# Performance work log

Measured on AMD Instinct MI355X. Metric: run time of the kernel, lower is better.

The kernel has to match this reference:

```python
import jax, jax.numpy as jnp
import numpy as np

# dims: batch, seq, d_model, mlp_width, num_experts, lora_rank
B, S, D, M, E, R = 4, 1024, 2048, 5632, 8, 16
LORA_ALPHA = 32
SCALING = LORA_ALPHA / R  # = 2.0


def setup_inputs() -> dict:
    key = jax.random.key(0)
    ks = jax.random.split(key, 13)
    s = 0.02
    f32 = jnp.float32
    return {
        'x':  jax.random.normal(ks[0], (B, S, D), f32),
        # router: nn.Linear(d_model, num_experts)
        'Wr': jax.random.normal(ks[1], (E, D), f32) * s,
        'br': jax.random.normal(ks[2], (E,), f32) * s,
        # frozen original MLP weights (torch Linear layout [out, in])
        'Wg': jax.random.normal(ks[3], (M, D), f32) * s,
        'Wu': jax.random.normal(ks[4], (M, D), f32) * s,
        'Wd': jax.random.normal(ks[5], (D, M), f32) * s,
        # shared LoRA A matrices [rank, fan_in]
        'Ag': jax.random.normal(ks[6], (R, D), f32) * s,
        'Au': jax.random.normal(ks[7], (R, D), f32) * s,
        'Ad': jax.random.normal(ks[8], (R, M), f32) * s,
        # per-expert LoRA B matrices [E, fan_out, rank] (zero-init in the
        # original; randomized here so gradients/outputs are non-trivial)
        'Bg': jax.random.normal(ks[9], (E, M, R), f32) * s,
        'Bu': jax.random.normal(ks[10], (E, M, R), f32) * s,
        'Bd': jax.random.normal(ks[11], (E, D, R), f32) * s,
    }


def _lora_moe_dense(x, W, A, Bexp, routing):
    """Dense MoE LoRA: original_proj(x) + sum_e routing[...,e] * (x @ A^T @ B_e^T) * scaling.
    x: [b,s,in], W: [out,in], A: [r,in], Bexp: [E,out,r], routing: [b,s,E].
    Identical math to stacking all experts then weighted-summing, but the
    shared A lets us weight the tiny [b,s,E,r] hidden instead of [b,s,E,out].
    """
    orig = jnp.einsum('bsi,oi->bso', x, W)
    h = jnp.einsum('bsi,ri->bsr', x, A)            # shared low-rank hidden
    hw = jnp.einsum('bsr,bse->bser', h, routing)   # routing-weighted hidden
    lora = jnp.einsum('bser,eor->bso', hw, Bexp) * SCALING
    return orig + lora


def reference(x, Wr, br, Wg, Wu, Wd, Ag, Au, Ad, Bg, Bu, Bd):
    logits = jnp.einsum('bsd,ed->bse', x, Wr) + br
    routing = jax.nn.softmax(logits, axis=-1)
    idx = jnp.argmax(routing, axis=-1)
    y_hard = jax.nn.one_hot(idx, E, dtype=logits.dtype)
    # straight-through expert choice
    expert_choice = y_hard - jax.lax.stop_gradient(routing) + routing
    gate = _lora_moe_dense(x, Wg, Ag, Bg, routing)
    up = _lora_moe_dense(x, Wu, Au, Bu, routing)
    h = jax.nn.silu(gate) * up  # LLaMA-style SwiGLU act_fn
    out = _lora_moe_dense(h, Wd, Ad, Bd, routing)
    return out, routing, expert_choice
```

## Files before the change

### kernel.cpp

```cpp
#include <hip/hip_runtime.h>

#define DEV __device__ __forceinline__

typedef unsigned short u16;
typedef __bf16 bf16x8 __attribute__((ext_vector_type(8)));
typedef float f32x4 __attribute__((ext_vector_type(4)));

static DEV u16 f2bf(float f) {
    union { float f; unsigned u; } v; v.f = f;
    unsigned r = v.u + 0x7fffu + ((v.u >> 16) & 1u);
    return (u16)(r >> 16);
}
static DEV float bf2f(u16 u) {
    union { unsigned u; float f; } v; v.u = ((unsigned)u) << 16;
    return v.f;
}
static DEV void g2l16(const u16* g, u16* l) {
    __builtin_amdgcn_global_load_lds(
        (const __attribute__((address_space(1))) void*)g,
        (__attribute__((address_space(3))) void*)l, 16, 0, 0);
}


__global__ __launch_bounds__(256) void k_conv(
    const float* __restrict__ Wg, const float* __restrict__ Wu, const float* __restrict__ Wd,
    const float* __restrict__ Bg, const float* __restrict__ Bu, const float* __restrict__ Bd,
    u16* __restrict__ Wg16, u16* __restrict__ Wu16, u16* __restrict__ Wd16,
    u16* __restrict__ Bgx, u16* __restrict__ Bux, u16* __restrict__ Bdx)
{
    const long long NW = 2883584;
    const long long NB = 180224;
    const long long ND = 65536;
    long long gid = (long long)blockIdx.x * 256 + threadIdx.x;
    if (gid < 3 * NW) {
        const float* s; u16* d; long long g = gid;
        if (g < NW)           { s = Wg; d = Wg16; }
        else if (g < 2 * NW)  { s = Wu; d = Wu16; g -= NW; }
        else                  { s = Wd; d = Wd16; g -= 2 * NW; }
        float4 v = *(const float4*)(s + g * 4);
        ushort4 o; o.x = f2bf(v.x); o.y = f2bf(v.y); o.z = f2bf(v.z); o.w = f2bf(v.w);
        *(ushort4*)(d + g * 4) = o;
    } else {
        long long g = gid - 3 * NW;
        const float* s; u16* d; int nr;
        if (g < NB)               { s = Bg; d = Bgx; nr = 5632; }
        else if (g < 2 * NB)      { s = Bu; d = Bux; nr = 5632; g -= NB; }
        else if (g < 2 * NB + ND) { s = Bd; d = Bdx; nr = 2048; g -= 2 * NB; }
        else return;
        int n = (int)(g >> 5);
        int j0 = ((int)g & 31) * 4;
        int e = j0 >> 4, r0 = j0 & 15;
        float4 v = *(const float4*)&s[((size_t)e * nr + n) * 16 + r0];
        ushort4 o; o.x = f2bf(v.x); o.y = f2bf(v.y); o.z = f2bf(v.z); o.w = f2bf(v.w);
        *(ushort4*)&d[(size_t)n * 128 + j0] = o;
    }
}

__global__ __launch_bounds__(256) void k_router(
    const float* __restrict__ x, const float* __restrict__ Wr,
    const float* __restrict__ Ag, const float* __restrict__ Au,
    u16* __restrict__ x16, float* __restrict__ fin1)
{
    __shared__ float xs[64][65];
    __shared__ float wsm[40][64];
    const int rb = blockIdx.x, ksp = blockIdx.y;
    const int row0 = rb * 64;
    const int t = threadIdx.x;
    const int rloc = t & 63, og = t >> 6;
    float acc[10];
#pragma unroll
    for (int o = 0; o < 10; ++o) acc[o] = 0.f;

    for (int c4 = 0; c4 < 4; ++c4) {
        const int k0 = ksp * 256 + c4 * 64;
        __syncthreads();
#pragma unroll
        for (int i = 0; i < 4; ++i) {
            int idx = t + i * 256;
            int r = idx >> 4, c = (idx & 15) * 4;
            float4 v = *(const float4*)&x[(size_t)(row0 + r) * 2048 + k0 + c];
            xs[r][c + 0] = v.x; xs[r][c + 1] = v.y; xs[r][c + 2] = v.z; xs[r][c + 3] = v.w;
            ushort4 o; o.x = f2bf(v.x); o.y = f2bf(v.y); o.z = f2bf(v.z); o.w = f2bf(v.w);
            *(ushort4*)&x16[(size_t)(row0 + r) * 2048 + k0 + c] = o;
        }
#pragma unroll
        for (int i = 0; i < 3; ++i) {
            int idx = t + i * 256;
            if (idx < 640) {
                int r = idx >> 4, c = (idx & 15) * 4;
                const float* src = (r < 8) ? (Wr + (size_t)r * 2048)
                                : (r < 24) ? (Ag + (size_t)(r - 8) * 2048)
                                           : (Au + (size_t)(r - 24) * 2048);
                float4 v = *(const float4*)&src[k0 + c];
                wsm[r][c + 0] = v.x; wsm[r][c + 1] = v.y; wsm[r][c + 2] = v.z; wsm[r][c + 3] = v.w;
            }
        }
        __syncthreads();
#pragma unroll
        for (int k = 0; k < 64; ++k) {
            float xv = xs[rloc][k];
#pragma unroll
            for (int o = 0; o < 10; ++o) acc[o] += xv * wsm[og * 10 + o][k];
        }
    }
    float* dst = fin1 + ((size_t)ksp * 4096 + row0 + rloc) * 40 + og * 10;
#pragma unroll
    for (int o = 0; o < 10; ++o) dst[o] = acc[o];
}

__global__ __launch_bounds__(256) void k_fin1(
    const float* __restrict__ fin1, const float* __restrict__ br,
    float* __restrict__ routing_ws, float* __restrict__ out_rt, float* __restrict__ out_ec,
    u16* __restrict__ hwg, u16* __restrict__ hwu)
{
    const int row = blockIdx.x * 256 + threadIdx.x;
    float s[40];
#pragma unroll
    for (int j = 0; j < 40; ++j) s[j] = 0.f;
    for (int p = 0; p < 8; ++p) {
        const float* src = fin1 + ((size_t)p * 4096 + row) * 40;
#pragma unroll
        for (int j = 0; j < 40; ++j) s[j] += src[j];
    }
    float lg[8]; float m = -1e30f;
#pragma unroll
    for (int e = 0; e < 8; ++e) { lg[e] = s[e] + br[e]; m = fmaxf(m, lg[e]); }
    float ex[8]; float sum = 0.f;
#pragma unroll
    for (int e = 0; e < 8; ++e) { ex[e] = expf(lg[e] - m); sum += ex[e]; }
    float r8[8];
#pragma unroll
    for (int e = 0; e < 8; ++e) r8[e] = ex[e] / sum;
    int best = 0;
#pragma unroll
    for (int e = 1; e < 8; ++e) if (r8[e] > r8[best]) best = e;
#pragma unroll
    for (int e = 0; e < 8; ++e) {
        routing_ws[(size_t)row * 8 + e] = r8[e];
        out_rt[(size_t)row * 8 + e] = r8[e];
        float yh = (e == best) ? 1.f : 0.f;
        out_ec[(size_t)row * 8 + e] = (yh - r8[e]) + r8[e];
    }
#pragma unroll
    for (int e = 0; e < 8; ++e) {
        float re = r8[e];
#pragma unroll
        for (int rk = 0; rk < 16; ++rk) {
            hwg[(size_t)row * 128 + e * 16 + rk] = f2bf(2.f * s[8 + rk] * re);
            hwu[(size_t)row * 128 + e * 16 + rk] = f2bf(2.f * s[24 + rk] * re);
        }
    }
}

__global__ __launch_bounds__(256, 3) void k_gemm(
    const u16* __restrict__ A0, int lda0, const u16* __restrict__ A1,
    const u16* __restrict__ B0, int ldb0, const u16* __restrict__ B1,
    int Ksplit, int nkt, int MODE,
    float* __restrict__ outF, u16* __restrict__ outH, int ldc)
{
    __shared__ u16 As[128 * 64];
    __shared__ u16 Bs[128 * 64];
    const int t = threadIdx.x;
    const int lane = t & 63, wid = t >> 6;
    const int wr = wid >> 1, wc = wid & 1;
    const int row0 = blockIdx.x * 128, col0 = blockIdx.y * 128;

    f32x4 acc[4][4];
    const f32x4 zf = {0.f, 0.f, 0.f, 0.f};
#pragma unroll
    for (int i = 0; i < 4; ++i)
#pragma unroll
        for (int j = 0; j < 4; ++j) acc[i][j] = zf;

    for (int kt = 0; kt < nkt; ++kt) {
        const int k0 = kt * 64;
        const bool p2 = (k0 >= Ksplit);
        const u16* aS = p2 ? A1 : A0; const int aLd = p2 ? 128 : lda0; const int aC = p2 ? (k0 - Ksplit) : k0;
        const u16* bS = p2 ? B1 : B0; const int bLd = p2 ? 128 : ldb0; const int bC = p2 ? (k0 - Ksplit) : k0;
        __syncthreads();
#pragma unroll
        for (int i = 0; i < 4; ++i) {
            int idx = i * 256 + t;
            int r = idx >> 3, c = (idx & 7) * 8;
            g2l16(aS + (size_t)(row0 + r) * aLd + aC + c, &As[idx * 8]);
        }
#pragma unroll
        for (int i = 0; i < 4; ++i) {
            int idx = i * 256 + t;
            int r = idx >> 3, c = (idx & 7) * 8;
            g2l16(bS + (size_t)(col0 + r) * bLd + bC + c, &Bs[idx * 8]);
        }
        __syncthreads();
#pragma unroll
        for (int ks = 0; ks < 2; ++ks) {
            bf16x8 af[4], bfr[4];
#pragma unroll
            for (int fm = 0; fm < 4; ++fm)
                af[fm] = *(const bf16x8*)&As[(wr * 64 + fm * 16 + (lane & 15)) * 64 + ks * 32 + (lane >> 4) * 8];
#pragma unroll
            for (int fn = 0; fn < 4; ++fn)
                bfr[fn] = *(const bf16x8*)&Bs[(wc * 64 + fn * 16 + (lane & 15)) * 64 + ks * 32 + (lane >> 4) * 8];
#pragma unroll
            for (int fm = 0; fm < 4; ++fm)
#pragma unroll
                for (int fn = 0; fn < 4; ++fn)
                    acc[fm][fn] = __builtin_amdgcn_mfma_f32_16x16x32_bf16(af[fm], bfr[fn], acc[fm][fn], 0, 0, 0);
        }
    }

#pragma unroll
    for (int fm = 0; fm < 4; ++fm) {
#pragma unroll
        for (int fn = 0; fn < 4; ++fn) {
            const int col = col0 + wc * 64 + fn * 16 + (lane & 15);
            const int rowb = row0 + wr * 64 + fm * 16 + ((lane >> 4) << 2);
            f32x4 v = acc[fm][fn];
            if (MODE == 0) {
#pragma unroll
                for (int j = 0; j < 4; ++j) outF[(size_t)(rowb + j) * ldc + col] = v[j];
            } else if (MODE == 1) {
#pragma unroll
                for (int j = 0; j < 4; ++j) outH[(size_t)(rowb + j) * ldc + col] = f2bf(v[j]);
            } else {
#pragma unroll
                for (int j = 0; j < 4; ++j) {
                    size_t o = (size_t)(rowb + j) * ldc + col;
                    float g = bf2f(outH[o]);
                    float sg = g / (1.f + __expf(-g));
                    outH[o] = f2bf(sg * v[j]);
                }
            }
        }
    }
}

__global__ __launch_bounds__(256) void k_hd(
    const u16* __restrict__ h, const float* __restrict__ Ad, float* __restrict__ fin2)
{
    __shared__ float hs[64][65];
    __shared__ float as2[16][64];
    const int rb = blockIdx.x, ksp = blockIdx.y;
    const int row0 = rb * 64;
    const int t = threadIdx.x;
    const int rloc = t & 63, og = t >> 6;
    float acc[4] = {0.f, 0.f, 0.f, 0.f};
    for (int c4 = 0; c4 < 11; ++c4) {
        const int k0 = ksp * 704 + c4 * 64;
        __syncthreads();
#pragma unroll
        for (int i = 0; i < 4; ++i) {
            int idx = t + i * 256;
            int r = idx >> 4, cc = (idx & 15) * 4;
            ushort4 v = *(const ushort4*)&h[(size_t)(row0 + r) * 5632 + k0 + cc];
            hs[r][cc + 0] = bf2f(v.x); hs[r][cc + 1] = bf2f(v.y);
            hs[r][cc + 2] = bf2f(v.z); hs[r][cc + 3] = bf2f(v.w);
        }
        {
            int r = t >> 4, cc = (t & 15) * 4;
            float4 w = *(const float4*)&Ad[(size_t)r * 5632 + k0 + cc];
            as2[r][cc + 0] = w.x; as2[r][cc + 1] = w.y; as2[r][cc + 2] = w.z; as2[r][cc + 3] = w.w;
        }
        __syncthreads();
#pragma unroll
        for (int k = 0; k < 64; ++k) {
            float hv = hs[rloc][k];
#pragma unroll
            for (int o = 0; o < 4; ++o) acc[o] += hv * as2[og * 4 + o][k];
        }
    }
    float* dst = fin2 + ((size_t)ksp * 4096 + row0 + rloc) * 16 + og * 4;
#pragma unroll
    for (int o = 0; o < 4; ++o) dst[o] = acc[o];
}

__global__ __launch_bounds__(256) void k_fin2(
    const float* __restrict__ fin2, const float* __restrict__ routing_ws, u16* __restrict__ hwd)
{
    const int row = blockIdx.x * 256 + threadIdx.x;
    float hd[16];
#pragma unroll
    for (int j = 0; j < 16; ++j) hd[j] = 0.f;
    for (int p = 0; p < 8; ++p) {
        const float* src = fin2 + ((size_t)p * 4096 + row) * 16;
#pragma unroll
        for (int j = 0; j < 16; ++j) hd[j] += src[j];
    }
#pragma unroll
    for (int e = 0; e < 8; ++e) {
        float re = routing_ws[(size_t)row * 8 + e];
#pragma unroll
        for (int rk = 0; rk < 16; ++rk)
            hwd[(size_t)row * 128 + e * 16 + rk] = f2bf(2.f * hd[rk] * re);
    }
}

extern "C" void kernel_launch(void* const* d_in, const int* in_sizes, int n_in,
                              void* d_out, int out_size, void* d_ws, size_t ws_size,
                              hipStream_t stream)
{
    (void)in_sizes; (void)n_in; (void)out_size; (void)ws_size;
    const float* x  = (const float*)d_in[0];
    const float* Wr = (const float*)d_in[1];
    const float* br = (const float*)d_in[2];
    const float* Wg = (const float*)d_in[3];
    const float* Wu = (const float*)d_in[4];
    const float* Wd = (const float*)d_in[5];
    const float* Ag = (const float*)d_in[6];
    const float* Au = (const float*)d_in[7];
    const float* Ad = (const float*)d_in[8];
    const float* Bg = (const float*)d_in[9];
    const float* Bu = (const float*)d_in[10];
    const float* Bd = (const float*)d_in[11];

    float* outp   = (float*)d_out;
    float* out_rt = outp + 8388608;
    float* out_ec = out_rt + 32768;

    char* p = (char*)d_ws;
    auto carve = [&](size_t n) -> char* { char* r = p; p += (n + 255) & ~(size_t)255; return r; };
    u16*   x16        = (u16*)carve(16777216);
    u16*   hwg        = (u16*)carve(1048576);
    u16*   hwu        = (u16*)carve(1048576);
    u16*   hwd        = (u16*)carve(1048576);
    float* routing_ws = (float*)carve(131072);
    float* fin1       = (float*)carve(5242880);
    float* fin2       = (float*)carve(2097152);
    u16*   Wg16       = (u16*)carve(23068672);
    u16*   Wu16       = (u16*)carve(23068672);
    u16*   Wd16       = (u16*)carve(23068672);
    u16*   Bgx        = (u16*)carve(1441792);
    u16*   Bux        = (u16*)carve(1441792);
    u16*   Bdx        = (u16*)carve(524288);
    u16*   hbuf       = (u16*)carve(46137344);

    k_conv<<<dim3(35456), dim3(256), 0, stream>>>(Wg, Wu, Wd, Bg, Bu, Bd,
                                                  Wg16, Wu16, Wd16, Bgx, Bux, Bdx);
    k_router<<<dim3(64, 8), dim3(256), 0, stream>>>(x, Wr, Ag, Au, x16, fin1);
    k_fin1<<<dim3(16), dim3(256), 0, stream>>>(fin1, br, routing_ws, out_rt, out_ec, hwg, hwu);
    k_gemm<<<dim3(32, 44), dim3(256), 0, stream>>>(x16, 2048, hwg, Wg16, 2048, Bgx,
                                                   2048, 34, 1, (float*)nullptr, hbuf, 5632);
    k_gemm<<<dim3(32, 44), dim3(256), 0, stream>>>(x16, 2048, hwu, Wu16, 2048, Bux,
                                                   2048, 34, 2, (float*)nullptr, hbuf, 5632);
    k_hd<<<dim3(64, 8), dim3(256), 0, stream>>>(hbuf, Ad, fin2);
    k_fin2<<<dim3(16), dim3(256), 0, stream>>>(fin2, routing_ws, hwd);
    k_gemm<<<dim3(32, 16), dim3(256), 0, stream>>>(hbuf, 5632, hwd, Wd16, 5632, Bdx,
                                                   5632, 90, 0, outp, (u16*)nullptr, 2048);
}
```

Before: 539.1 us.

## Replace GEMM with 256x256 double-buffered pipelined kernel, merge gate/up, split-K down

Replaces the 128x128 single-buffered GEMM with a 512-thread 256x256 tile kernel. It double-buffers LDS with XOR-swizzled global-to-LDS loads, interleaves MFMA clusters with barriers and priority hints, and remaps blocks with an XCD-aware swizzle. The gate and up projections run in one launch writing separate buffers, and SiLU*up moves into the k_hd pass, which writes h back over the gate buffer. The down projection uses split-K into two partials summed by a new reduce kernel, to fill more CUs. This costs an extra 46MB buffer and extra read/write traffic for the separate gate/up outputs and the reduction.

```diff
diff --git a/kernel.cpp b/kernel.cpp
--- a/kernel.cpp
+++ b/kernel.cpp
@@ -20,6 +20,22 @@
         (const __attribute__((address_space(1))) void*)g,
         (__attribute__((address_space(3))) void*)l, 16, 0, 0);
 }
+
+#define BAR()    do { __builtin_amdgcn_s_barrier(); __builtin_amdgcn_sched_barrier(0); } while (0)
+#define WAITV(N) asm volatile("s_waitcnt vmcnt(" #N ")" ::: "memory")
+
+#define MM16(A, B, FMO, FNO) do {                                            \
+    __builtin_amdgcn_s_setprio(1);                                           \
+    _Pragma("unroll")                                                        \
+    for (int fm_ = 0; fm_ < 4; ++fm_)                                        \
+      _Pragma("unroll")                                                      \
+      for (int fn_ = 0; fn_ < 2; ++fn_)                                      \
+        _Pragma("unroll")                                                    \
+        for (int ks_ = 0; ks_ < 2; ++ks_)                                    \
+          acc[(FMO) + fm_][(FNO) + fn_] = __builtin_amdgcn_mfma_f32_16x16x32_bf16( \
+              A[fm_][ks_], B[fn_][ks_], acc[(FMO) + fm_][(FNO) + fn_], 0, 0, 0); \
+    __builtin_amdgcn_s_setprio(0);                                           \
+} while (0)
 
 
 __global__ __launch_bounds__(256) void k_conv(
@@ -152,90 +168,138 @@
     }
 }
 
-__global__ __launch_bounds__(256, 3) void k_gemm(
-    const u16* __restrict__ A0, int lda0, const u16* __restrict__ A1,
-    const u16* __restrict__ B0, int ldb0, const u16* __restrict__ B1,
-    int Ksplit, int nkt, int MODE,
-    float* __restrict__ outF, u16* __restrict__ outH, int ldc)
-{
-    __shared__ u16 As[128 * 64];
-    __shared__ u16 Bs[128 * 64];
+template<int MODE>
+__global__ __launch_bounds__(512, 2) void k_gemm8(
+    const u16* __restrict__ A0, int lda0,
+    const u16* __restrict__ A1g, const u16* __restrict__ A1u,
+    const u16* __restrict__ B0g, int ldb0, const u16* __restrict__ B0u,
+    const u16* __restrict__ B1g, const u16* __restrict__ B1u,
+    int Ksplit,
+    float* __restrict__ outF0, float* __restrict__ outF1,
+    u16* __restrict__ outHg, u16* __restrict__ outHu,
+    int nbm, int nbn)
+{
+    __shared__ u16 lds[65536];
     const int t = threadIdx.x;
-    const int lane = t & 63, wid = t >> 6;
-    const int wr = wid >> 1, wc = wid & 1;
-    const int row0 = blockIdx.x * 128, col0 = blockIdx.y * 128;
-
-    f32x4 acc[4][4];
+    const int nwg = (int)gridDim.x;
+    const int orig = (int)blockIdx.x;
+    const int sw = (orig & 7) * (nwg >> 3) + (orig >> 3);
+    const int bm = sw % nbm; const int rest = sw / nbm;
+    const int bn = rest % nbn; const int z = rest / nbn;
+
+    const int row0 = bm * 256, col0 = bn * 256;
+    int ktb, ntl;
+    if (MODE == 0) { ktb = z ? 46 : 0; ntl = z ? 44 : 46; }
+    else           { ktb = 0;          ntl = 34; }
+    const int kend = ktb + ntl;
+    const u16* A1 = (MODE == 1 && z) ? A1u : A1g;
+    const u16* B0 = (MODE == 1 && z) ? B0u : B0g;
+    const u16* B1 = (MODE == 1 && z) ? B1u : B1g;
+
+    const int lane = t & 63, lr = lane & 15, lg = lane >> 4;
+    const int wid = t >> 6, wr = wid >> 2, wcol = wid & 3;
+    const int arow = wr * 128 + lr;
+    const int brow = wcol * 64 + lr;
+    const int sa = (arow & 7) << 3;
+    const int sb = (brow & 7) << 3;
+
+    auto stg = [&](int kt, int h, int isB) {
+        const int k0 = kt * 64;
+        const u16* s; int ld; int kc;
+        if (isB) { if (k0 >= Ksplit) { s = B1; ld = 128; kc = k0 - Ksplit; } else { s = B0; ld = ldb0; kc = k0; } }
+        else     { if (k0 >= Ksplit) { s = A1; ld = 128; kc = k0 - Ksplit; } else { s = A0; ld = lda0; kc = k0; } }
+        const int r0 = isB ? col0 : row0;
+        u16* base = lds + (isB ? 32768 : 0) + (kt & 1) * 16384;
+#pragma unroll
+        for (int j = 0; j < 2; ++j) {
+            const int o = h * 16384 + j * 8192 + t * 16;
+            const int r = o >> 7;
+            const int cb = (o & 127) ^ ((r & 7) << 4);
+            g2l16(s + (size_t)(r0 + r) * ld + kc + (cb >> 1), (u16*)((char*)base + o));
+        }
+    };
+    auto rdA = [&](int buf, int fb, bf16x8 a[4][2]) {
+#pragma unroll
+        for (int fm = 0; fm < 4; ++fm)
+#pragma unroll
+            for (int ks = 0; ks < 2; ++ks)
+                a[fm][ks] = *(const bf16x8*)&lds[buf * 16384 + (arow + (fb + fm) * 16) * 64
+                                                 + (((ks << 5) | (lg << 3)) ^ sa)];
+    };
+    auto rdB = [&](int buf, int fb, bf16x8 b[2][2]) {
+#pragma unroll
+        for (int fn = 0; fn < 2; ++fn)
+#pragma unroll
+            for (int ks = 0; ks < 2; ++ks)
+                b[fn][ks] = *(const bf16x8*)&lds[32768 + buf * 16384 + (brow + (fb + fn) * 16) * 64
+                                                 + (((ks << 5) | (lg << 3)) ^ sb)];
+    };
+
+    f32x4 acc[8][4];
     const f32x4 zf = {0.f, 0.f, 0.f, 0.f};
 #pragma unroll
-    for (int i = 0; i < 4; ++i)
+    for (int i = 0; i < 8; ++i)
 #pragma unroll
         for (int j = 0; j < 4; ++j) acc[i][j] = zf;
 
-    for (int kt = 0; kt < nkt; ++kt) {
-        const int k0 = kt * 64;
-        const bool p2 = (k0 >= Ksplit);
-        const u16* aS = p2 ? A1 : A0; const int aLd = p2 ? 128 : lda0; const int aC = p2 ? (k0 - Ksplit) : k0;
-        const u16* bS = p2 ? B1 : B0; const int bLd = p2 ? 128 : ldb0; const int bC = p2 ? (k0 - Ksplit) : k0;
-        __syncthreads();
-#pragma unroll
-        for (int i = 0; i < 4; ++i) {
-            int idx = i * 256 + t;
-            int r = idx >> 3, c = (idx & 7) * 8;
-            g2l16(aS + (size_t)(row0 + r) * aLd + aC + c, &As[idx * 8]);
-        }
-#pragma unroll
-        for (int i = 0; i < 4; ++i) {
-            int idx = i * 256 + t;
-            int r = idx >> 3, c = (idx & 7) * 8;
-            g2l16(bS + (size_t)(col0 + r) * bLd + bC + c, &Bs[idx * 8]);
-        }
-        __syncthreads();
-#pragma unroll
-        for (int ks = 0; ks < 2; ++ks) {
-            bf16x8 af[4], bfr[4];
-#pragma unroll
-            for (int fm = 0; fm < 4; ++fm)
-                af[fm] = *(const bf16x8*)&As[(wr * 64 + fm * 16 + (lane & 15)) * 64 + ks * 32 + (lane >> 4) * 8];
-#pragma unroll
-            for (int fn = 0; fn < 4; ++fn)
-                bfr[fn] = *(const bf16x8*)&Bs[(wc * 64 + fn * 16 + (lane & 15)) * 64 + ks * 32 + (lane >> 4) * 8];
-#pragma unroll
-            for (int fm = 0; fm < 4; ++fm)
-#pragma unroll
-                for (int fn = 0; fn < 4; ++fn)
-                    acc[fm][fn] = __builtin_amdgcn_mfma_f32_16x16x32_bf16(af[fm], bfr[fn], acc[fm][fn], 0, 0, 0);
-        }
-    }
-
-#pragma unroll
-    for (int fm = 0; fm < 4; ++fm) {
+    stg(ktb, 0, 0); stg(ktb, 1, 0);
+    stg(ktb, 0, 1); stg(ktb, 1, 1);
+    stg(ktb + 1, 0, 1); stg(ktb + 1, 1, 1);
+    WAITV(4);
+    BAR();
+
+    const int ni = ntl >> 1;
+    for (int i = 0; i < ni; ++i) {
+        const int kt0 = ktb + 2 * i, kt1 = kt0 + 1;
+        const bool s2 = (kt0 + 2 < kend), s3 = (kt1 + 2 < kend);
+        bf16x8 alo[4][2], ahi[4][2], b01[2][2], b23[2][2];
+        rdA(0, 0, alo); rdB(0, 0, b01);
+        stg(kt1, 0, 0);
+        BAR(); MM16(alo, b01, 0, 0); BAR();
+        rdB(0, 2, b23);
+        stg(kt1, 1, 0);
+        BAR(); MM16(alo, b23, 0, 2); BAR();
+        rdA(0, 4, ahi);
+        if (s2) stg(kt0 + 2, 0, 1);
+        BAR(); MM16(ahi, b01, 4, 0); BAR();
+        if (s2) { stg(kt0 + 2, 1, 1); WAITV(4); } else { WAITV(0); }
+        BAR(); MM16(ahi, b23, 4, 2); BAR();
+        rdA(1, 0, alo); rdB(1, 0, b01);
+        if (s2) stg(kt0 + 2, 0, 0);
+        BAR(); MM16(alo, b01, 0, 0); BAR();
+        rdB(1, 2, b23);
+        if (s2) stg(kt0 + 2, 1, 0);
+        BAR(); MM16(alo, b23, 0, 2); BAR();
+        rdA(1, 4, ahi);
+        if (s3) stg(kt1 + 2, 0, 1);
+        BAR(); MM16(ahi, b01, 4, 0); BAR();
+        if (s3) { stg(kt1 + 2, 1, 1); WAITV(4); } else { WAITV(0); }
+        BAR(); MM16(ahi, b23, 4, 2); BAR();
+    }
+
+#pragma unroll
+    for (int fm = 0; fm < 8; ++fm) {
 #pragma unroll
         for (int fn = 0; fn < 4; ++fn) {
-            const int col = col0 + wc * 64 + fn * 16 + (lane & 15);
-            const int rowb = row0 + wr * 64 + fm * 16 + ((lane >> 4) << 2);
+            const int r = row0 + wr * 128 + fm * 16 + lg * 4;
+            const int c = col0 + wcol * 64 + fn * 16 + lr;
             f32x4 v = acc[fm][fn];
-            if (MODE == 0) {
-#pragma unroll
-                for (int j = 0; j < 4; ++j) outF[(size_t)(rowb + j) * ldc + col] = v[j];
-            } else if (MODE == 1) {
-#pragma unroll
-                for (int j = 0; j < 4; ++j) outH[(size_t)(rowb + j) * ldc + col] = f2bf(v[j]);
+            if constexpr (MODE == 0) {
+                float* out = z ? outF1 : outF0;
+#pragma unroll
+                for (int j = 0; j < 4; ++j) out[(size_t)(r + j) * 2048 + c] = v[j];
             } else {
-#pragma unroll
-                for (int j = 0; j < 4; ++j) {
-                    size_t o = (size_t)(rowb + j) * ldc + col;
-                    float g = bf2f(outH[o]);
-                    float sg = g / (1.f + __expf(-g));
-                    outH[o] = f2bf(sg * v[j]);
-                }
+                u16* out = z ? outHu : outHg;
+#pragma unroll
+                for (int j = 0; j < 4; ++j) out[(size_t)(r + j) * 5632 + c] = f2bf(v[j]);
             }
         }
     }
 }
 
 __global__ __launch_bounds__(256) void k_hd(
-    const u16* __restrict__ h, const float* __restrict__ Ad, float* __restrict__ fin2)
+    u16* __restrict__ g, const u16* __restrict__ u,
+    const float* __restrict__ Ad, float* __restrict__ fin2)
 {
     __shared__ float hs[64][65];
     __shared__ float as2[16][64];
@@ -251,9 +315,17 @@
         for (int i = 0; i < 4; ++i) {
             int idx = t + i * 256;
             int r = idx >> 4, cc = (idx & 15) * 4;
-            ushort4 v = *(const ushort4*)&h[(size_t)(row0 + r) * 5632 + k0 + cc];
-            hs[r][cc + 0] = bf2f(v.x); hs[r][cc + 1] = bf2f(v.y);
-            hs[r][cc + 2] = bf2f(v.z); hs[r][cc + 3] = bf2f(v.w);
+            size_t go = (size_t)(row0 + r) * 5632 + k0 + cc;
+            ushort4 gv = *(const ushort4*)&g[go];
+            ushort4 uv = *(const ushort4*)&u[go];
+            float h0, h1, h2, h3;
+            { float gg = bf2f(gv.x); h0 = gg / (1.f + __expf(-gg)) * bf2f(uv.x); }
+            { float gg = bf2f(gv.y); h1 = gg / (1.f + __expf(-gg)) * bf2f(uv.y); }
+            { float gg = bf2f(gv.z); h2 = gg / (1.f + __expf(-gg)) * bf2f(uv.z); }
+            { float gg = bf2f(gv.w); h3 = gg / (1.f + __expf(-gg)) * bf2f(uv.w); }
+            hs[r][cc + 0] = h0; hs[r][cc + 1] = h1; hs[r][cc + 2] = h2; hs[r][cc + 3] = h3;
+            ushort4 hv; hv.x = f2bf(h0); hv.y = f2bf(h1); hv.z = f2bf(h2); hv.w = f2bf(h3);
+            *(ushort4*)&g[go] = hv;
         }
         {
             int r = t >> 4, cc = (t & 15) * 4;
@@ -292,6 +364,16 @@
         for (int rk = 0; rk < 16; ++rk)
             hwd[(size_t)row * 128 + e * 16 + rk] = f2bf(2.f * hd[rk] * re);
     }
+}
+
+__global__ __launch_bounds__(256) void k_reduce(
+    float* __restrict__ o, const float* __restrict__ p1)
+{
+    size_t i = ((size_t)blockIdx.x * 256 + threadIdx.x) * 4;
+    float4 a = *(const float4*)&o[i];
+    float4 b = *(const float4*)&p1[i];
+    float4 r; r.x = a.x + b.x; r.y = a.y + b.y; r.z = a.z + b.z; r.w = a.w + b.w;
+    *(float4*)&o[i] = r;
 }
 
 extern "C" void kernel_launch(void* const* d_in, const int* in_sizes, int n_in,
@@ -331,18 +413,21 @@
     u16*   Bgx        = (u16*)carve(1441792);
     u16*   Bux        = (u16*)carve(1441792);
     u16*   Bdx        = (u16*)carve(524288);
-    u16*   hbuf       = (u16*)carve(46137344);
+    u16*   gbuf       = (u16*)carve(46137344);
+    u16*   ubuf       = (u16*)carve(46137344);
+    float* part1      = (float*)ubuf;
 
     k_conv<<<dim3(35456), dim3(256), 0, stream>>>(Wg, Wu, Wd, Bg, Bu, Bd,
                                                   Wg16, Wu16, Wd16, Bgx, Bux, Bdx);
     k_router<<<dim3(64, 8), dim3(256), 0, stream>>>(x, Wr, Ag, Au, x16, fin1);
     k_fin1<<<dim3(16), dim3(256), 0, stream>>>(fin1, br, routing_ws, out_rt, out_ec, hwg, hwu);
-    k_gemm<<<dim3(32, 44), dim3(256), 0, stream>>>(x16, 2048, hwg, Wg16, 2048, Bgx,
-                                                   2048, 34, 1, (float*)nullptr, hbuf, 5632);
-    k_gemm<<<dim3(32, 44), dim3(256), 0, stream>>>(x16, 2048, hwu, Wu16, 2048, Bux,
-                                                   2048, 34, 2, (float*)nullptr, hbuf, 5632);
-    k_hd<<<dim3(64, 8), dim3(256), 0, stream>>>(hbuf, Ad, fin2);
+    k_gemm8<1><<<dim3(704), dim3(512), 0, stream>>>(
+        x16, 2048, hwg, hwu, Wg16, 2048, Wu16, Bgx, Bux,
+        2048, (float*)nullptr, (float*)nullptr, gbuf, ubuf, 16, 22);
+    k_hd<<<dim3(64, 8), dim3(256), 0, stream>>>(gbuf, ubuf, Ad, fin2);
     k_fin2<<<dim3(16), dim3(256), 0, stream>>>(fin2, routing_ws, hwd);
-    k_gemm<<<dim3(32, 16), dim3(256), 0, stream>>>(hbuf, 5632, hwd, Wd16, 5632, Bdx,
-                                                   5632, 90, 0, outp, (u16*)nullptr, 2048);
-}
+    k_gemm8<0><<<dim3(256), dim3(512), 0, stream>>>(
+        gbuf, 5632, hwd, hwd, Wd16, 5632, Wd16, Bdx, Bdx,
+        5632, outp, part1, (u16*)nullptr, (u16*)nullptr, 16, 8);
+    k_reduce<<<dim3(8192), dim3(256), 0, stream>>>(outp, part1);
+}
```

Measured after the change: 472.5 us. 1.14x faster.
